# Optimization experiments

Hardware: AMD Instinct MI355X
Metric: run time of the kernel (lower is better)

Reference implementation:

```python
import jax, jax.numpy as jnp
import numpy as np

T, B, N, D, H = 12, 32, 64, 2, 128
HID, HEAD = 32, 4          # GATBlock n_hid, n_head; HEAD*HID == H
M = N * (N - 1)            # edge rows per get_graph
N_ACT = N - 1              # active nodes per batch row


def _make_graph():
    rec = np.zeros((M, N), np.float32)
    snd = np.zeros((M, N), np.float32)
    k = np.arange(N_ACT * N_ACT)
    ii = np.repeat(np.arange(N_ACT), N_ACT)
    jj = np.tile(np.arange(N_ACT), N_ACT)
    snd[k, ii] = 1.0
    rec[k, jj] = 1.0
    return rec, snd


def setup_inputs() -> dict:
    key = jax.random.key(0)
    ks = jax.random.split(key, 16)
    rec, snd = _make_graph()
    inp = {
        "inputs": jax.random.normal(ks[0], (T, B, N, D), jnp.float32),
        "hidden": jax.random.normal(ks[1], (B, N, H), jnp.float32),
        "rel_rec": jnp.asarray(np.broadcast_to(rec, (B, M, N)).copy()),
        "rel_send": jnp.asarray(np.broadcast_to(snd, (B, M, N)).copy()),
        # GATBlock rn1: fc1(D->HID), fc2(2*HID->HEAD)
        "rn1_W1": jax.random.normal(ks[2], (HID, D)) * 0.1,
        "rn1_b1": jnp.zeros((HID,)),
        "rn1_W2": jax.random.normal(ks[3], (HEAD, 2 * HID)) * 0.1,
        "rn1_b2": jnp.zeros((HEAD,)),
        # GATBlock rn2: fc1(H->HID), fc2(2*HID->HEAD)
        "rn2_W1": jax.random.normal(ks[4], (HID, H)) * 0.1,
        "rn2_b1": jnp.zeros((HID,)),
        "rn2_W2": jax.random.normal(ks[5], (HEAD, 2 * HID)) * 0.1,
        "rn2_b2": jnp.zeros((HEAD,)),
        # GRUCell(H, H)
        "gru_Wih": jax.random.normal(ks[6], (3 * H, H)) * 0.05,
        "gru_Whh": jax.random.normal(ks[7], (3 * H, H)) * 0.05,
        "gru_bih": jnp.zeros((3 * H,)),
        "gru_bhh": jnp.zeros((3 * H,)),
        # out Linear(H, D)
        "out_W": jax.random.normal(ks[8], (D, H)) * 0.1,
        "out_b": jnp.zeros((D,)),
    }
    return inp


def _gat_block(x_in, rel_rec, rel_send, W1, b1, W2, b2):
    # x_in: B x N x Din
    x = x_in @ W1.T + b1                                   # B,N,HID
    s = jnp.einsum('bmn,bnd->bmd', rel_send, x)            # B,M,HID (senders)
    r = jnp.einsum('bmn,bnd->bmd', rel_rec, x)             # B,M,HID (receivers)
    a = jax.nn.elu(jnp.concatenate([s, r], -1) @ W2.T + b2)  # B,M,HEAD
    # per-receiving-node masked softmax over the edge dim (edge2node)
    m = rel_rec[..., None] > 0                             # B,M,N,1
    logits = jnp.where(m, a[:, :, None, :], -jnp.inf)      # B,M,N,HEAD
    mx = jnp.max(logits, axis=1, keepdims=True)
    mx = jnp.where(jnp.isfinite(mx), mx, 0.0)
    e = jnp.where(m, jnp.exp(logits - mx), 0.0)
    denom = jnp.sum(e, axis=1, keepdims=True)
    att = e / jnp.where(denom > 0, denom, 1.0)             # B,M,N,HEAD
    # weighted scatter-sum: outer(att_edge, sender_feat) summed per node
    out = jnp.einsum('bmnh,bmd->bnhd', att, s)             # B,N,HEAD,HID
    Bn, Nn = x_in.shape[0], x_in.shape[1]
    return jax.nn.elu(out.reshape(Bn, Nn, HEAD * HID))     # B,N,H


def _gru_cell(x, h, Wih, Whh, bih, bhh):
    gi = x @ Wih.T + bih
    gh = h @ Whh.T + bhh
    i_r, i_z, i_n = jnp.split(gi, 3, axis=-1)
    h_r, h_z, h_n = jnp.split(gh, 3, axis=-1)
    r = jax.nn.sigmoid(i_r + h_r)
    z = jax.nn.sigmoid(i_z + h_z)
    n = jnp.tanh(i_n + r * h_n)
    return (1.0 - z) * n + z * h


def reference(inputs, hidden, rel_rec, rel_send,
              rn1_W1, rn1_b1, rn1_W2, rn1_b2,
              rn2_W1, rn2_b1, rn2_W2, rn2_b2,
              gru_Wih, gru_Whh, gru_bih, gru_bhh,
              out_W, out_b):
    def step(h, x_t):
        x = _gat_block(x_t, rel_rec, rel_send, rn1_W1, rn1_b1, rn1_W2, rn1_b2)
        h = _gru_cell(x, h, gru_Wih, gru_Whh, gru_bih, gru_bhh)
        h = _gat_block(h, rel_rec, rel_send, rn2_W1, rn2_b1, rn2_W2, rn2_b2)
        return h, None
    h_final, _ = jax.lax.scan(step, hidden, inputs)
    pred = h_final @ out_W.T + out_b                       # B,N,D
    return pred
```

## Files before the change

### kernel.cpp

```cpp
#include <hip/hip_runtime.h>


#define T_   12
#define B_   32
#define N_   64
#define D_   2
#define H_   128
#define HID_ 32
#define HEAD_ 4
#define NA_  63

__device__ __forceinline__ float eluf(float x){ return x>0.f ? x : expm1f(x); }

#define OFF_H    0u
#define OFF_X1   262144u
#define OFF_PS1  1048576u
#define OFF_PR1  1146880u
#define OFF_XG   1245184u
#define OFF_X2   4390912u
#define OFF_PS2  4456448u
#define OFF_PR2  4464640u
#define OFF_WT   OFF_X1
#define OFF_GI   4472832u
#define WS_NEED_A ((4472832ull + 9437184ull) * 4ull)

__global__ void gat1_fc(const float* __restrict__ inp, const float* __restrict__ W1,
                        const float* __restrict__ b1, const float* __restrict__ W2,
                        const float* __restrict__ b2,
                        float* __restrict__ x1_all, float* __restrict__ ps_all,
                        float* __restrict__ pr_all){
  int grp = blockIdx.x;
  int tid = threadIdx.x;
  __shared__ float sx1[N_*HID_];
  __shared__ float sW1[HID_*D_];
  __shared__ float sb1[HID_];
  __shared__ float sW2[HEAD_*2*HID_];
  __shared__ float sxin[N_*D_];
  if(tid < 64)  sW1[tid] = W1[tid];
  if(tid < 32)  sb1[tid] = b1[tid];
  sW2[tid] = W2[tid];
  if(tid < 128) sxin[tid] = inp[grp*N_*D_ + tid];
  __syncthreads();
  for(int o = tid; o < N_*HID_; o += 256){
    int n = o >> 5, k = o & 31;
    float v = sb1[k] + sxin[n*2]*sW1[k*2] + sxin[n*2+1]*sW1[k*2+1];
    sx1[o] = v;
    x1_all[grp*N_*HID_ + o] = v;
  }
  __syncthreads();
  for(int p = tid; p < N_*8; p += 256){
    int n = p >> 3, q = p & 7, hh = q & 3;
    const float* w  = sW2 + hh*64 + ((q < 4) ? 0 : 32);
    const float* xr = sx1 + n*32;
    float acc = (q < 4) ? b2[hh] : 0.f;
    #pragma unroll
    for(int c = 0; c < 32; c++) acc += xr[c]*w[c];
    if(q < 4) ps_all[grp*N_*HEAD_ + n*4 + hh] = acc;
    else      pr_all[grp*N_*HEAD_ + n*4 + hh] = acc;
  }
}

__global__ void prep_wt(const float* __restrict__ Wih, const float* __restrict__ Whh,
                        float* __restrict__ wtb){
  int idx = blockIdx.x*256 + threadIdx.x;
  int k4 = idx / 768, j = idx - k4*768;
  const float* src = (j < 384) ? (Wih + (size_t)j*H_) : (Whh + (size_t)(j-384)*H_);
  ((float4*)wtb)[idx] = ((const float4*)src)[k4];
}

__global__ __launch_bounds__(256) void gat_att_big2(const float* __restrict__ x1,
    const float* __restrict__ ps, const float* __restrict__ pr,
    float* __restrict__ out){
  int blk = blockIdx.x, g = blk >> 1, dh = blk & 1, tid = threadIdx.x;
  __shared__ float sX[N_*HID_];
  __shared__ float sPs[N_*HEAD_];
  __shared__ float sPr[N_*HEAD_];
  {
    const float4* xs = (const float4*)(x1 + (size_t)g*(N_*HID_));
    ((float4*)sX)[tid]       = xs[tid];
    ((float4*)sX)[tid + 256] = xs[tid + 256];
    sPs[tid] = ps[g*(N_*HEAD_) + tid];
    sPr[tid] = pr[g*(N_*HEAD_) + tid];
  }
  __syncthreads();
  float* outg = out + (size_t)g*(N_*H_);
  if(tid < NA_*HEAD_){
    int r = tid, hh = r & 3;
    float prv = sPr[r];
    float tmax = -1e30f;
    for(int i = 0; i < NA_; i++) tmax = fmaxf(tmax, sPs[i*4 + hh]);
    float m = eluf(tmax + prv);
    float4 acc[4];
    #pragma unroll
    for(int k = 0; k < 4; k++) acc[k] = make_float4(0.f,0.f,0.f,0.f);
    float s = 0.f;
    #pragma unroll 3
    for(int i = 0; i < NA_; i++){
      float tt = sPs[i*4 + hh] + prv;
      float v = tt > 0.f ? tt : expm1f(tt);
      float p = expf(v - m);
      s += p;
      const float4* sxp = (const float4*)&sX[i*32 + dh*16];
      #pragma unroll
      for(int k = 0; k < 4; k++){
        float4 xv = sxp[k];
        acc[k].x += p*xv.x; acc[k].y += p*xv.y;
        acc[k].z += p*xv.z; acc[k].w += p*xv.w;
      }
    }
    float inv = 1.f/s;
    float4* orow = (float4*)(outg + (r>>2)*H_ + hh*32 + dh*16);
    #pragma unroll
    for(int k = 0; k < 4; k++){
      float4 o;
      o.x = eluf(acc[k].x*inv); o.y = eluf(acc[k].y*inv);
      o.z = eluf(acc[k].z*inv); o.w = eluf(acc[k].w*inv);
      orow[k] = o;
    }
  } else {
    int hh = tid - NA_*HEAD_;
    float4 z4 = make_float4(0.f,0.f,0.f,0.f);
    float4* zp = (float4*)(outg + NA_*H_ + hh*32 + dh*16);
    zp[0]=z4; zp[1]=z4; zp[2]=z4; zp[3]=z4;
  }
}

__global__ __launch_bounds__(256) void gi_gemm4(const float* __restrict__ xg,
    const float* __restrict__ wtb, float* __restrict__ gi){
  int tid = threadIdx.x;
  int r0 = blockIdx.x * 16;
  __shared__ __align__(16) float sxg[16][H_];
  ((float4*)sxg)[tid]       = ((const float4*)(xg + (size_t)r0*H_))[tid];
  ((float4*)sxg)[tid + 256] = ((const float4*)(xg + (size_t)r0*H_))[tid + 256];
  __syncthreads();
  int c = tid & 127, rh = (tid >> 7) * 8;
  const float4* wt4 = (const float4*)wtb;
  float ar[8]={0,0,0,0,0,0,0,0}, az[8]={0,0,0,0,0,0,0,0}, an[8]={0,0,0,0,0,0,0,0};
  #pragma unroll 2
  for(int k4 = 0; k4 < 32; k4++){
    float4 w0 = wt4[k4*768 + c];
    float4 w1 = wt4[k4*768 + 128 + c];
    float4 w2 = wt4[k4*768 + 256 + c];
    #pragma unroll
    for(int rr = 0; rr < 8; rr++){
      float4 xv = ((const float4*)sxg[rh + rr])[k4];
      ar[rr] += w0.x*xv.x + w0.y*xv.y + w0.z*xv.z + w0.w*xv.w;
      az[rr] += w1.x*xv.x + w1.y*xv.y + w1.z*xv.z + w1.w*xv.w;
      an[rr] += w2.x*xv.x + w2.y*xv.y + w2.z*xv.z + w2.w*xv.w;
    }
  }
  #pragma unroll
  for(int rr = 0; rr < 8; rr++){
    size_t base = (size_t)(r0 + rh + rr)*384;
    gi[base + c]       = ar[rr];
    gi[base + 128 + c] = az[rr];
    gi[base + 256 + c] = an[rr];
  }
}

__global__ __launch_bounds__(256) void gru_fc8(
    const float* __restrict__ gi, const float* __restrict__ hidden0, int t0,
    const float* __restrict__ x2prev, const float* __restrict__ psprev,
    const float* __restrict__ prprev,
    const float* __restrict__ wtb,
    const float* __restrict__ bih, const float* __restrict__ bhh,
    const float* __restrict__ W1, const float* __restrict__ b1,
    const float* __restrict__ W2, const float* __restrict__ b2,
    float* __restrict__ x2, float* __restrict__ ps2, float* __restrict__ pr2){
  int tid = threadIdx.x, blk = blockIdx.x;
  int g0 = blk*4, g = blk>>4, jbase = (blk&15)*4;
  __shared__ __align__(16) float sX[N_*HID_];
  __shared__ float sPs[N_*HEAD_];
  __shared__ __align__(16) float sh[4][H_];
  __shared__ __align__(16) float shn[4][H_];
  __shared__ float spart[2][12][H_];
  __shared__ float sx2[4][HID_];

  if(t0){
    if(tid < 128) ((float4*)sh)[tid] = ((const float4*)(hidden0 + (size_t)g0*H_))[tid];
  } else {
    ((float4*)sX)[tid]       = ((const float4*)(x2prev + (size_t)g*(N_*HID_)))[tid];
    ((float4*)sX)[tid + 256] = ((const float4*)(x2prev + (size_t)g*(N_*HID_)))[tid + 256];
    sPs[tid] = psprev[g*(N_*HEAD_) + tid];
  }
  __syncthreads();

  if(!t0){
    int rl = tid >> 4, l16 = tid & 15;
    int hh = rl & 3, jrow = rl >> 2;
    int jl = jbase + jrow;
    float prv = prprev[g*(N_*HEAD_) + jbase*4 + rl];
    float tmax = -1e30f;
    for(int i = 0; i < NA_; i++) tmax = fmaxf(tmax, sPs[i*4 + hh]);
    float m = eluf(tmax + prv);
    float a0 = 0.f, a1 = 0.f, s = 0.f;
    #pragma unroll 3
    for(int i = 0; i < NA_; i++){
      float tt = sPs[i*4 + hh] + prv;
      float v = tt > 0.f ? tt : expm1f(tt);
      float p = expf(v - m);
      s += p;
      const float2 xv = *(const float2*)&sX[i*32 + l16*2];
      a0 += p*xv.x; a1 += p*xv.y;
    }
    float inv = 1.f/s;
    float h0 = (jl == NA_) ? 0.f : eluf(a0*inv);
    float h1 = (jl == NA_) ? 0.f : eluf(a1*inv);
    sh[jrow][hh*32 + l16*2]     = h0;
    sh[jrow][hh*32 + l16*2 + 1] = h1;
  }
  __syncthreads();

  int c = tid & 127, rg = tid >> 7;
  {
    const float4* wt4 = (const float4*)wtb;
    float ar[4] = {0,0,0,0};
    float az[4] = {0,0,0,0};
    float an[4] = {0,0,0,0};
    #pragma unroll
    for(int kk = 0; kk < 16; kk++){
      int k4 = rg*16 + kk;
      const float4* wk = wt4 + (size_t)k4*768 + 384 + c;
      float4 wr_ = wk[0], wz_ = wk[128], wn_ = wk[256];
      #pragma unroll
      for(int r = 0; r < 4; r++){
        float4 hv = ((const float4*)sh[r])[k4];
        ar[r] += wr_.x*hv.x + wr_.y*hv.y + wr_.z*hv.z + wr_.w*hv.w;
        az[r] += wz_.x*hv.x + wz_.y*hv.y + wz_.z*hv.z + wz_.w*hv.w;
        an[r] += wn_.x*hv.x + wn_.y*hv.y + wn_.z*hv.z + wn_.w*hv.w;
      }
    }
    #pragma unroll
    for(int r = 0; r < 4; r++){
      spart[rg][r][c]     = ar[r];
      spart[rg][4 + r][c] = az[r];
      spart[rg][8 + r][c] = an[r];
    }
  }
  __syncthreads();

  {
    float bi_r = bih[c], bi_z = bih[c+H_], bi_n = bih[c+2*H_];
    float bh_r = bhh[c], bh_z = bhh[c+H_], bh_n = bhh[c+2*H_];
    int r0 = rg*2;
    #pragma unroll
    for(int rr = 0; rr < 2; rr++){
      int r = r0 + rr;
      float hr = spart[0][r][c]   + spart[1][r][c]   + bh_r;
      float hz = spart[0][4+r][c] + spart[1][4+r][c] + bh_z;
      float hn = spart[0][8+r][c] + spart[1][8+r][c] + bh_n;
      const float* gir = gi + (size_t)(g0+r)*384;
      float ir  = gir[c]     + bi_r;
      float iz  = gir[c+128] + bi_z;
      float in_ = gir[c+256] + bi_n;
      float rgt = 1.f/(1.f+expf(-(ir+hr)));
      float zgt = 1.f/(1.f+expf(-(iz+hz)));
      float ngt = tanhf(in_ + rgt*hn);
      shn[r][c] = (1.f-zgt)*ngt + zgt*sh[r][c];
    }
  }
  __syncthreads();

  if(tid < 128){
    int r = tid >> 5, jc = tid & 31;
    const float4* wrow = (const float4*)(W1 + (size_t)jc*H_);
    const float4* hnr = (const float4*)shn[r];
    float acc = b1[jc];
    #pragma unroll 8
    for(int k4 = 0; k4 < 32; k4++){
      float4 w = wrow[k4], hv = hnr[k4];
      acc += w.x*hv.x + w.y*hv.y + w.z*hv.z + w.w*hv.w;
    }
    sx2[r][jc] = acc;
    x2[(size_t)(g0+r)*HID_ + jc] = acc;
  }
  __syncthreads();
  if(tid < 32){
    int r = tid >> 3, q = tid & 7, hh = q & 3;
    int base = (q < 4) ? 0 : 32;
    float acc = (q < 4) ? b2[hh] : 0.f;
    #pragma unroll
    for(int cc = 0; cc < 32; cc++) acc += sx2[r][cc]*W2[hh*64 + base + cc];
    if(q < 4) ps2[(g0+r)*HEAD_ + hh] = acc;
    else      pr2[(g0+r)*HEAD_ + hh] = acc;
  }
}

__global__ __launch_bounds__(512) void gru_fc3(
    const float* __restrict__ xg, const float* __restrict__ h,
    const float* __restrict__ wtb,
    const float* __restrict__ bih, const float* __restrict__ bhh,
    const float* __restrict__ W1, const float* __restrict__ b1,
    const float* __restrict__ W2, const float* __restrict__ b2,
    float* __restrict__ x2, float* __restrict__ ps2, float* __restrict__ pr2){
  int tid = threadIdx.x;
  int g0 = blockIdx.x * 8;
  __shared__ __align__(16) float sx[8][H_];
  __shared__ __align__(16) float sh[8][H_];
  __shared__ __align__(16) float shn[8][H_];
  __shared__ float sx2[8][HID_];
  if(tid < 256) ((float4*)sx)[tid]     = ((const float4*)(xg + (size_t)g0*H_))[tid];
  else          ((float4*)sh)[tid-256] = ((const float4*)(h  + (size_t)g0*H_))[tid-256];
  __syncthreads();
  int c = tid & 127, rg = tid >> 7, r0 = rg*2;
  const float4* wt4 = (const float4*)wtb;
  const float4* xr0 = (const float4*)sx[r0];
  const float4* xr1 = (const float4*)sx[r0+1];
  const float4* hp0 = (const float4*)sh[r0];
  const float4* hp1 = (const float4*)sh[r0+1];
  float air[2]={0,0}, aiz[2]={0,0}, ain[2]={0,0};
  float ahr[2]={0,0}, ahz[2]={0,0}, ahn[2]={0,0};
  #pragma unroll 2
  for(int k4 = 0; k4 < 32; k4++){
    const float4* wk = wt4 + k4*768 + c;
    float4 w0 = wk[0],   w1 = wk[128], w2 = wk[256];
    float4 w3 = wk[384], w4 = wk[512], w5 = wk[640];
    float4 xv0 = xr0[k4], xv1 = xr1[k4];
    float4 hv0 = hp0[k4], hv1 = hp1[k4];
    air[0] += w0.x*xv0.x + w0.y*xv0.y + w0.z*xv0.z + w0.w*xv0.w;
    aiz[0] += w1.x*xv0.x + w1.y*xv0.y + w1.z*xv0.z + w1.w*xv0.w;
    ain[0] += w2.x*xv0.x + w2.y*xv0.y + w2.z*xv0.z + w2.w*xv0.w;
    ahr[0] += w3.x*hv0.x + w3.y*hv0.y + w3.z*hv0.z + w3.w*hv0.w;
    ahz[0] += w4.x*hv0.x + w4.y*hv0.y + w4.z*hv0.z + w4.w*hv0.w;
    ahn[0] += w5.x*hv0.x + w5.y*hv0.y + w5.z*hv0.z + w5.w*hv0.w;
    air[1] += w0.x*xv1.x + w0.y*xv1.y + w0.z*xv1.z + w0.w*xv1.w;
    aiz[1] += w1.x*xv1.x + w1.y*xv1.y + w1.z*xv1.z + w1.w*xv1.w;
    ain[1] += w2.x*xv1.x + w2.y*xv1.y + w2.z*xv1.z + w2.w*xv1.w;
    ahr[1] += w3.x*hv1.x + w3.y*hv1.y + w3.z*hv1.z + w3.w*hv1.w;
    ahz[1] += w4.x*hv1.x + w4.y*hv1.y + w4.z*hv1.z + w4.w*hv1.w;
    ahn[1] += w5.x*hv1.x + w5.y*hv1.y + w5.z*hv1.z + w5.w*hv1.w;
  }
  float bi_r = bih[c], bi_z = bih[c+H_], bi_n = bih[c+2*H_];
  float bh_r = bhh[c], bh_z = bhh[c+H_], bh_n = bhh[c+2*H_];
  #pragma unroll
  for(int rr = 0; rr < 2; rr++){
    float ir  = air[rr]+bi_r, iz = aiz[rr]+bi_z, in_ = ain[rr]+bi_n;
    float hr  = ahr[rr]+bh_r, hz = ahz[rr]+bh_z, hn  = ahn[rr]+bh_n;
    float rgt = 1.f/(1.f+expf(-(ir+hr)));
    float zgt = 1.f/(1.f+expf(-(iz+hz)));
    float ngt = tanhf(in_ + rgt*hn);
    shn[r0+rr][c] = (1.f-zgt)*ngt + zgt*sh[r0+rr][c];
  }
  __syncthreads();
  if(tid < 256){
    int r = tid >> 5, jc = tid & 31;
    const float4* wrow = (const float4*)(W1 + (size_t)jc*H_);
    const float4* hnr = (const float4*)shn[r];
    float acc = b1[jc];
    #pragma unroll 8
    for(int k4 = 0; k4 < 32; k4++){
      float4 w = wrow[k4], hv = hnr[k4];
      acc += w.x*hv.x + w.y*hv.y + w.z*hv.z + w.w*hv.w;
    }
    sx2[r][jc] = acc;
    x2[(size_t)(g0+r)*HID_ + jc] = acc;
  }
  __syncthreads();
  if(tid < 64){
    int r = tid >> 3, q = tid & 7, hh = q & 3;
    int base = (q < 4) ? 0 : 32;
    float acc = (q < 4) ? b2[hh] : 0.f;
    #pragma unroll
    for(int cc = 0; cc < 32; cc++) acc += sx2[r][cc]*W2[hh*64 + base + cc];
    if(q < 4) ps2[(g0+r)*HEAD_ + hh] = acc;
    else      pr2[(g0+r)*HEAD_ + hh] = acc;
  }
}

__global__ __launch_bounds__(128) void gat_att_sm(const float* __restrict__ x1,
    const float* __restrict__ ps, const float* __restrict__ pr,
    float* __restrict__ out){
  int bid = blockIdx.x;
  int g = bid >> 3, sub = bid & 7, rh = sub >> 2, dq = sub & 3;
  int tid = threadIdx.x;
  __shared__ float sX[N_*HID_];
  __shared__ float sPs[N_*HEAD_];
  __shared__ float sPr[N_*HEAD_];
  {
    const float4* xs = (const float4*)(x1 + (size_t)g*(N_*HID_));
    #pragma unroll
    for(int k = 0; k < 4; k++) ((float4*)sX)[tid + 128*k] = xs[tid + 128*k];
    sPs[tid]       = ps[g*(N_*HEAD_) + tid];
    sPs[tid + 128] = ps[g*(N_*HEAD_) + tid + 128];
    sPr[tid]       = pr[g*(N_*HEAD_) + tid];
    sPr[tid + 128] = pr[g*(N_*HEAD_) + tid + 128];
  }
  __syncthreads();
  float* outg = out + (size_t)g*(N_*H_);
  if(tid < 126){
    int r = rh*126 + tid;
    int hh = r & 3, j = r >> 2;
    float prv = sPr[r];
    float tmax = -1e30f;
    for(int i = 0; i < NA_; i++) tmax = fmaxf(tmax, sPs[i*4 + hh]);
    float m = eluf(tmax + prv);
    float4 a0 = make_float4(0.f,0.f,0.f,0.f), a1 = a0;
    float s = 0.f;
    #pragma unroll 3
    for(int i = 0; i < NA_; i++){
      float tt = sPs[i*4 + hh] + prv;
      float v = tt > 0.f ? tt : expm1f(tt);
      float p = expf(v - m);
      s += p;
      const float4* sxp = (const float4*)&sX[i*32 + dq*8];
      float4 x0 = sxp[0], x1v = sxp[1];
      a0.x += p*x0.x;  a0.y += p*x0.y;  a0.z += p*x0.z;  a0.w += p*x0.w;
      a1.x += p*x1v.x; a1.y += p*x1v.y; a1.z += p*x1v.z; a1.w += p*x1v.w;
    }
    float inv = 1.f/s;
    float4* orow = (float4*)(outg + (size_t)j*H_ + hh*32 + dq*8);
    float4 o0, o1;
    o0.x = eluf(a0.x*inv); o0.y = eluf(a0.y*inv);
    o0.z = eluf(a0.z*inv); o0.w = eluf(a0.w*inv);
    o1.x = eluf(a1.x*inv); o1.y = eluf(a1.y*inv);
    o1.z = eluf(a1.z*inv); o1.w = eluf(a1.w*inv);
    orow[0] = o0; orow[1] = o1;
  } else if(rh == 1){
    float4 z4 = make_float4(0.f,0.f,0.f,0.f);
    float4* zrow = (float4*)(outg + NA_*H_);
    int base = dq*8 + (tid-126)*4;
    #pragma unroll
    for(int k = 0; k < 4; k++) zrow[base + k] = z4;
  }
}

__global__ void final_k(const float* __restrict__ h, const float* __restrict__ oW,
                        const float* __restrict__ ob, float* __restrict__ out){
  int b = blockIdx.x, tid = threadIdx.x;
  int n = tid >> 1, d = tid & 1;
  const float* hr = h + (size_t)(b*N_ + n)*H_;
  float acc = ob[d];
  #pragma unroll 8
  for(int k = 0; k < H_; k++) acc += hr[k]*oW[d*H_ + k];
  out[(b*N_ + n)*D_ + d] = acc;
}

extern "C" void kernel_launch(void* const* d_in, const int* in_sizes, int n_in,
                              void* d_out, int out_size, void* d_ws, size_t ws_size,
                              hipStream_t stream){
  const float* inputs = (const float*)d_in[0];
  const float* hidden = (const float*)d_in[1];
  const float* rn1_W1 = (const float*)d_in[4];
  const float* rn1_b1 = (const float*)d_in[5];
  const float* rn1_W2 = (const float*)d_in[6];
  const float* rn1_b2 = (const float*)d_in[7];
  const float* rn2_W1 = (const float*)d_in[8];
  const float* rn2_b1 = (const float*)d_in[9];
  const float* rn2_W2 = (const float*)d_in[10];
  const float* rn2_b2 = (const float*)d_in[11];
  const float* gWih   = (const float*)d_in[12];
  const float* gWhh   = (const float*)d_in[13];
  const float* gbih   = (const float*)d_in[14];
  const float* gbhh   = (const float*)d_in[15];
  const float* oW     = (const float*)d_in[16];
  const float* ob     = (const float*)d_in[17];
  float* ws = (float*)d_ws;

  const int use_gi = (ws_size >= WS_NEED_A) ? 1 : 0;

  gat1_fc<<<T_*B_, 256, 0, stream>>>(inputs, rn1_W1, rn1_b1, rn1_W2, rn1_b2,
                                     ws + OFF_X1, ws + OFF_PS1, ws + OFF_PR1);
  gat_att_big2<<<T_*B_*2, 256, 0, stream>>>(ws + OFF_X1, ws + OFF_PS1, ws + OFF_PR1,
                                            ws + OFF_XG);
  prep_wt<<<96, 256, 0, stream>>>(gWih, gWhh, ws + OFF_WT);

  const float* xg0  = ws + OFF_XG;
  const float* wtbp = ws + OFF_WT;
  float* hb  = ws + OFF_H;

  if(use_gi){
    gi_gemm4<<<T_*B_*N_/16, 256, 0, stream>>>(xg0, wtbp, ws + OFF_GI);
    float* x2b[2] = {ws + OFF_X2,  ws + OFF_PS1};
    float* psb[2] = {ws + OFF_PS2, ws + OFF_PR1};
    float* prb[2] = {ws + OFF_PR2, ws + OFF_PR1 + 8192};
    for(int t = 0; t < T_; t++){
      int w = t & 1, rp = w ^ 1;
      gru_fc8<<<B_*N_/4, 256, 0, stream>>>(ws + OFF_GI + (size_t)t*B_*N_*384,
                                           hidden, (t == 0) ? 1 : 0,
                                           x2b[rp], psb[rp], prb[rp],
                                           wtbp, gbih, gbhh,
                                           rn2_W1, rn2_b1, rn2_W2, rn2_b2,
                                           x2b[w], psb[w], prb[w]);
    }
    gat_att_sm<<<B_*8, 128, 0, stream>>>(x2b[1], psb[1], prb[1], hb);
  } else {
    float* x2p = ws + OFF_X2;
    float* psp = ws + OFF_PS2;
    float* prp = ws + OFF_PR2;
    for(int t = 0; t < T_; t++){
      const float* hsrc = (t == 0) ? hidden : hb;
      gru_fc3<<<B_*N_/8, 512, 0, stream>>>(xg0 + (size_t)t*B_*N_*H_, hsrc,
                                           wtbp, gbih, gbhh,
                                           rn2_W1, rn2_b1, rn2_W2, rn2_b2,
                                           x2p, psp, prp);
      gat_att_sm<<<B_*8, 128, 0, stream>>>(x2p, psp, prp, hb);
    }
  }
  final_k<<<B_, 128, 0, stream>>>(hb, oW, ob, (float*)d_out);
}
```

Before: 460.7 us.

## Fuse layer-1 GAT attention with input-gate GEMM via shared memory

Replaces the separate layer-1 attention kernel and the gi GEMM with one kernel. Each block computes the attention output for a graph into shared memory and then multiplies it by the GRU input weights to write gi for half the gate columns. This removes the global round trip of the xg intermediate and one launch. In exchange the attention work is done twice, once per column half, and the block needs more shared memory, which may lower occupancy.

```diff
diff --git a/kernel.cpp b/kernel.cpp
--- a/kernel.cpp
+++ b/kernel.cpp
@@ -68,6 +68,92 @@
   ((float4*)wtb)[idx] = ((const float4*)src)[k4];
 }
 
+__global__ __launch_bounds__(256) void gat_att_gi(const float* __restrict__ x1,
+    const float* __restrict__ ps, const float* __restrict__ pr,
+    const float* __restrict__ wtb, float* __restrict__ gi){
+  int blk = blockIdx.x, g = blk >> 1, ch = blk & 1, tid = threadIdx.x;
+  __shared__ float sX[N_*HID_];
+  __shared__ float sPs[N_*HEAD_];
+  __shared__ float sPr[N_*HEAD_];
+  __shared__ __align__(16) float sxg[N_][H_];
+  {
+    const float4* xs = (const float4*)(x1 + (size_t)g*(N_*HID_));
+    ((float4*)sX)[tid]       = xs[tid];
+    ((float4*)sX)[tid + 256] = xs[tid + 256];
+    sPs[tid] = ps[g*(N_*HEAD_) + tid];
+    sPr[tid] = pr[g*(N_*HEAD_) + tid];
+  }
+  __syncthreads();
+  if(tid < NA_*HEAD_){
+    int r = tid, hh = r & 3, j = r >> 2;
+    float prv = sPr[r];
+    float tmax = -1e30f;
+    for(int i = 0; i < NA_; i++) tmax = fmaxf(tmax, sPs[i*4 + hh]);
+    float m = eluf(tmax + prv);
+    float4 acc[8];
+    #pragma unroll
+    for(int k = 0; k < 8; k++) acc[k] = make_float4(0.f,0.f,0.f,0.f);
+    float s = 0.f;
+    #pragma unroll 3
+    for(int i = 0; i < NA_; i++){
+      float tt = sPs[i*4 + hh] + prv;
+      float v = tt > 0.f ? tt : expm1f(tt);
+      float p = expf(v - m);
+      s += p;
+      const float4* sxp = (const float4*)&sX[i*32];
+      #pragma unroll
+      for(int k = 0; k < 8; k++){
+        float4 xv = sxp[k];
+        acc[k].x += p*xv.x; acc[k].y += p*xv.y;
+        acc[k].z += p*xv.z; acc[k].w += p*xv.w;
+      }
+    }
+    float inv = 1.f/s;
+    float4* orow = (float4*)&sxg[j][hh*32];
+    #pragma unroll
+    for(int k = 0; k < 8; k++){
+      float4 o;
+      o.x = eluf(acc[k].x*inv); o.y = eluf(acc[k].y*inv);
+      o.z = eluf(acc[k].z*inv); o.w = eluf(acc[k].w*inv);
+      orow[k] = o;
+    }
+  } else {
+    float4 z4 = make_float4(0.f,0.f,0.f,0.f);
+    float4* zp = (float4*)sxg[NA_];
+    for(int k = tid - NA_*HEAD_; k < 32; k += 4) zp[k] = z4;
+  }
+  __syncthreads();
+  {
+    int c = ch*64 + (tid & 63), rh8 = (tid >> 6) * 8;
+    const float4* wt4 = (const float4*)wtb;
+    #pragma unroll
+    for(int pass = 0; pass < 2; pass++){
+      int rbase = pass*32 + rh8;
+      float ar[8]={0,0,0,0,0,0,0,0}, az[8]={0,0,0,0,0,0,0,0}, an[8]={0,0,0,0,0,0,0,0};
+      #pragma unroll 2
+      for(int k4 = 0; k4 < 32; k4++){
+        float4 w0 = wt4[k4*768 + c];
+        float4 w1 = wt4[k4*768 + 128 + c];
+        float4 w2 = wt4[k4*768 + 256 + c];
+        #pragma unroll
+        for(int rr = 0; rr < 8; rr++){
+          float4 xv = ((const float4*)sxg[rbase + rr])[k4];
+          ar[rr] += w0.x*xv.x + w0.y*xv.y + w0.z*xv.z + w0.w*xv.w;
+          az[rr] += w1.x*xv.x + w1.y*xv.y + w1.z*xv.z + w1.w*xv.w;
+          an[rr] += w2.x*xv.x + w2.y*xv.y + w2.z*xv.z + w2.w*xv.w;
+        }
+      }
+      #pragma unroll
+      for(int rr = 0; rr < 8; rr++){
+        size_t base = (size_t)(g*N_ + rbase + rr)*384;
+        gi[base + c]       = ar[rr];
+        gi[base + 128 + c] = az[rr];
+        gi[base + 256 + c] = an[rr];
+      }
+    }
+  }
+}
+
 __global__ __launch_bounds__(256) void gat_att_big2(const float* __restrict__ x1,
     const float* __restrict__ ps, const float* __restrict__ pr,
     float* __restrict__ out){
@@ -122,39 +208,6 @@
     float4 z4 = make_float4(0.f,0.f,0.f,0.f);
     float4* zp = (float4*)(outg + NA_*H_ + hh*32 + dh*16);
     zp[0]=z4; zp[1]=z4; zp[2]=z4; zp[3]=z4;
-  }
-}
-
-__global__ __launch_bounds__(256) void gi_gemm4(const float* __restrict__ xg,
-    const float* __restrict__ wtb, float* __restrict__ gi){
-  int tid = threadIdx.x;
-  int r0 = blockIdx.x * 16;
-  __shared__ __align__(16) float sxg[16][H_];
-  ((float4*)sxg)[tid]       = ((const float4*)(xg + (size_t)r0*H_))[tid];
-  ((float4*)sxg)[tid + 256] = ((const float4*)(xg + (size_t)r0*H_))[tid + 256];
-  __syncthreads();
-  int c = tid & 127, rh = (tid >> 7) * 8;
-  const float4* wt4 = (const float4*)wtb;
-  float ar[8]={0,0,0,0,0,0,0,0}, az[8]={0,0,0,0,0,0,0,0}, an[8]={0,0,0,0,0,0,0,0};
-  #pragma unroll 2
-  for(int k4 = 0; k4 < 32; k4++){
-    float4 w0 = wt4[k4*768 + c];
-    float4 w1 = wt4[k4*768 + 128 + c];
-    float4 w2 = wt4[k4*768 + 256 + c];
-    #pragma unroll
-    for(int rr = 0; rr < 8; rr++){
-      float4 xv = ((const float4*)sxg[rh + rr])[k4];
-      ar[rr] += w0.x*xv.x + w0.y*xv.y + w0.z*xv.z + w0.w*xv.w;
-      az[rr] += w1.x*xv.x + w1.y*xv.y + w1.z*xv.z + w1.w*xv.w;
-      an[rr] += w2.x*xv.x + w2.y*xv.y + w2.z*xv.z + w2.w*xv.w;
-    }
-  }
-  #pragma unroll
-  for(int rr = 0; rr < 8; rr++){
-    size_t base = (size_t)(r0 + rh + rr)*384;
-    gi[base + c]       = ar[rr];
-    gi[base + 128 + c] = az[rr];
-    gi[base + 256 + c] = an[rr];
   }
 }
 
@@ -460,16 +513,13 @@
 
   gat1_fc<<<T_*B_, 256, 0, stream>>>(inputs, rn1_W1, rn1_b1, rn1_W2, rn1_b2,
                                      ws + OFF_X1, ws + OFF_PS1, ws + OFF_PR1);
-  gat_att_big2<<<T_*B_*2, 256, 0, stream>>>(ws + OFF_X1, ws + OFF_PS1, ws + OFF_PR1,
-                                            ws + OFF_XG);
-  prep_wt<<<96, 256, 0, stream>>>(gWih, gWhh, ws + OFF_WT);
-
-  const float* xg0  = ws + OFF_XG;
-  const float* wtbp = ws + OFF_WT;
-  float* hb  = ws + OFF_H;
+  float* hb = ws + OFF_H;
 
   if(use_gi){
-    gi_gemm4<<<T_*B_*N_/16, 256, 0, stream>>>(xg0, wtbp, ws + OFF_GI);
+    float* wtbp = ws + OFF_XG;
+    prep_wt<<<96, 256, 0, stream>>>(gWih, gWhh, wtbp);
+    gat_att_gi<<<T_*B_*2, 256, 0, stream>>>(ws + OFF_X1, ws + OFF_PS1, ws + OFF_PR1,
+                                            wtbp, ws + OFF_GI);
     float* x2b[2] = {ws + OFF_X2,  ws + OFF_PS1};
     float* psb[2] = {ws + OFF_PS2, ws + OFF_PR1};
     float* prb[2] = {ws + OFF_PR2, ws + OFF_PR1 + 8192};
@@ -484,6 +534,11 @@
     }
     gat_att_sm<<<B_*8, 128, 0, stream>>>(x2b[1], psb[1], prb[1], hb);
   } else {
+    gat_att_big2<<<T_*B_*2, 256, 0, stream>>>(ws + OFF_X1, ws + OFF_PS1, ws + OFF_PR1,
+                                              ws + OFF_XG);
+    prep_wt<<<96, 256, 0, stream>>>(gWih, gWhh, ws + OFF_WT);
+    const float* xg0  = ws + OFF_XG;
+    const float* wtbp = ws + OFF_WT;
     float* x2p = ws + OFF_X2;
     float* psp = ws + OFF_PS2;
     float* prp = ws + OFF_PR2;
```

Result: no change. 469.3 us (+1.9%).
